# Optimization experiments

Measured on AMD Instinct MI355X. Metric: run time of the kernel, lower is better.

Reference implementation:

```python
import jax, jax.numpy as jnp
import numpy as np

K = 1024
D = 64
BETA = 0.25


def setup_inputs() -> dict:
    key = jax.random.key(0)
    k1, k2 = jax.random.split(key)
    latents = jax.random.normal(k1, (32, 64, 64, 64), dtype=jnp.float32)  # [B, C=D, H, W]
    # embedding init: uniform(-1/K, 1/K)
    embedding = jax.random.uniform(k2, (K, D), dtype=jnp.float32, minval=-1.0 / K, maxval=1.0 / K)
    return {"latents": latents, "embedding": embedding}


def reference(latents, embedding):
    # [B, D, H, W] -> [B, H, W, D]
    x = jnp.transpose(latents, (0, 2, 3, 1))
    shp = x.shape
    flat = x.reshape(-1, D)  # [N, D]

    dist = (jnp.sum(flat ** 2, axis=1, keepdims=True)
            + jnp.sum(embedding ** 2, axis=1)
            - 2.0 * flat @ embedding.T)  # [N, K]
    inds = jnp.argmin(dist, axis=1)  # [N]

    quantized = embedding[inds].reshape(shp)  # gather == one-hot @ embedding

    commitment_loss = jnp.mean((jax.lax.stop_gradient(quantized) - x) ** 2)
    embedding_loss = jnp.mean((quantized - jax.lax.stop_gradient(x)) ** 2)
    vq_loss = commitment_loss * BETA + embedding_loss

    # straight-through estimator
    quantized = x + jax.lax.stop_gradient(quantized - x)
    out = jnp.transpose(quantized, (0, 3, 1, 2))  # back to [B, D, H, W]
    return out, vq_loss
```

## Files before the change

kernel.cpp:

```cpp
#include <hip/hip_runtime.h>
#include <hip/hip_bf16.h>


#define HW 4096
#define OUTELEMS 8388608

typedef __attribute__((ext_vector_type(8))) short bf16x8;
typedef __attribute__((ext_vector_type(4))) float f32x4;

static __device__ __forceinline__ short f2bf(float f) {
    union { __hip_bfloat16 h; short s; } u;
    u.h = __float2bfloat16(f);
    return u.s;
}


__global__ __launch_bounds__(256) void prep_kernel(const float* __restrict__ emb,
                                                   short* __restrict__ Ebf,
                                                   float* __restrict__ en1,
                                                   float* __restrict__ embT,
                                                   float* __restrict__ loss) {
    int code = blockIdx.x * 4 + (threadIdx.x >> 6);
    int d = threadIdx.x & 63;
    float v = emb[code * 64 + d];
    int g = d >> 3, j = d & 7;
    Ebf[code * 64 + ((g + code) & 7) * 8 + j] = f2bf(-2.0f * v);
    embT[d * 1024 + code] = v;
    float s = v * v;
#pragma unroll
    for (int off = 32; off > 0; off >>= 1) s += __shfl_xor(s, off, 64);
    if (d == 0) en1[code] = 1.0f + s;
    if (blockIdx.x == 0 && threadIdx.x == 0) *loss = 0.0f;
}

__global__ __launch_bounds__(512, 4) void argmin_kernel(
        const float* __restrict__ lat, const short* __restrict__ Ebf,
        const float* __restrict__ en1, int* __restrict__ idx_out,
        float* __restrict__ loss) {
    __shared__ __align__(16) char sbuf[65536];
    const int tid  = threadIdx.x;
    const int wave = tid >> 6;
    const int lane = tid & 63;
    const int n    = lane & 15;
    const int quad = lane >> 4;

    const int g0 = blockIdx.x * 256;
    const int b  = g0 >> 12;
    const int m0 = (g0 & 4095) + wave * 32;
    const float* latb = lat + (size_t)b * 262144;
    const char* EbfB = (const char*)Ebf;

    f32x4 stg[4];
#pragma unroll
    for (int r = 0; r < 4; ++r)
        stg[r] = *(const f32x4*)(EbfB + r * 8192 + tid * 16);

    bf16x8 bfr[2][2];
    float xnorm[2];
    {
        float xv[32];
#pragma unroll
        for (int s = 0; s < 2; ++s) {
            const float* xp = latb + m0 + s * 16 + n;
#pragma unroll
            for (int j = 0; j < 8; ++j) {
                xv[s * 16 + j]     = xp[(quad * 8 + j) * HW];
                xv[s * 16 + 8 + j] = xp[(32 + quad * 8 + j) * HW];
            }
        }
#pragma unroll
        for (int s = 0; s < 2; ++s) {
            float xs = 0.0f; bf16x8 f0, f1;
#pragma unroll
            for (int j = 0; j < 8; ++j) {
                float x0 = xv[s * 16 + j], x1 = xv[s * 16 + 8 + j];
                xs += x0 * x0 + x1 * x1;
                f0[j] = f2bf(x0); f1[j] = f2bf(x1);
            }
            bfr[s][0] = f0; bfr[s][1] = f1; xnorm[s] = xs;
        }
    }

#pragma unroll
    for (int r = 0; r < 4; ++r)
        *(f32x4*)(sbuf + r * 8192 + tid * 16) = stg[r];
    __syncthreads();

    const f32x4* en1v = (const f32x4*)en1;
    unsigned emin[2] = {0xFFFFFFFFu, 0xFFFFFFFFu};
    const int slot0 = ((quad + n) & 7) * 16;
    const int slot1 = ((quad + 4 + n) & 7) * 16;

    for (int c = 0; c < 4; ++c) {
        const char* bufc = sbuf + (c & 1) * 32768;
        char* bufn = sbuf + ((c + 1) & 1) * 32768;
        if (c < 3) {
            const char* src = EbfB + (c + 1) * 32768;
#pragma unroll
            for (int r = 0; r < 4; ++r)
                stg[r] = *(const f32x4*)(src + r * 8192 + tid * 16);
        }
        const char* arow0 = bufc + n * 128 + slot0;
        const char* arow1 = bufc + n * 128 + slot1;
#pragma unroll 4
        for (int ctl = 0; ctl < 16; ++ctl) {
            bf16x8 a0 = *(const bf16x8*)(arow0 + ctl * 2048);
            bf16x8 a1 = *(const bf16x8*)(arow1 + ctl * 2048);
            f32x4 en4 = en1v[c * 64 + ctl * 4 + quad];
            f32x4 acc[2];
#pragma unroll
            for (int s = 0; s < 2; ++s)
                acc[s] = __builtin_amdgcn_mfma_f32_16x16x32_bf16(a0, bfr[s][0], en4, 0, 0, 0);
#pragma unroll
            for (int s = 0; s < 2; ++s)
                acc[s] = __builtin_amdgcn_mfma_f32_16x16x32_bf16(a1, bfr[s][1], acc[s], 0, 0, 0);
            const unsigned cb = c * 256 + ctl * 16 + quad * 4;
#pragma unroll
            for (int s = 0; s < 2; ++s) {
#pragma unroll
                for (int r = 0; r < 4; ++r) {
                    unsigned enc = (__float_as_uint(acc[s][r]) & 0xFFFFFC00u) | (cb + r);
                    emin[s] = enc < emin[s] ? enc : emin[s];
                }
            }
        }
        if (c < 3) {
#pragma unroll
            for (int r = 0; r < 4; ++r)
                *(f32x4*)(bufn + r * 8192 + tid * 16) = stg[r];
        }
        __syncthreads();
    }

#pragma unroll
    for (int off = 16; off <= 32; off <<= 1) {
#pragma unroll
        for (int s = 0; s < 2; ++s) {
            unsigned eo = (unsigned)__shfl_xor((int)emin[s], off, 64);
            float xo = __shfl_xor(xnorm[s], off, 64);
            emin[s] = eo < emin[s] ? eo : emin[s];
            xnorm[s] += xo;
        }
    }
    if (quad == 0) {
#pragma unroll
        for (int s = 0; s < 2; ++s)
            idx_out[b * HW + m0 + s * 16 + n] = (int)(emin[s] & 1023u);
    }
    float contrib = 0.0f;
#pragma unroll
    for (int s = 0; s < 2; ++s)
        contrib += __uint_as_float(emin[s] & 0xFFFFFC00u) - 1.0f + xnorm[s];
#pragma unroll
    for (int off = 32; off > 0; off >>= 1) contrib += __shfl_xor(contrib, off, 64);
    float* wsum = (float*)sbuf;
    if (lane == 0) wsum[wave] = contrib;
    __syncthreads();
    if (tid == 0) {
        float t = 0.0f;
#pragma unroll
        for (int w = 0; w < 8; ++w) t += wsum[w];
        atomicAdd(loss, t * (1.25f / (8388608.0f * 4.0f)));
    }
}

__global__ __launch_bounds__(256) void gather_kernel(const float* __restrict__ embT,
                                                     const int* __restrict__ idxb,
                                                     float* __restrict__ out) {
    int id = blockIdx.x * 256 + threadIdx.x;
    int m  = id & 4095;
    int d  = (id >> 12) & 63;
    int bbase = (id >> 18) << 12;
    int code = idxb[bbase + m];
    out[id] = embT[(d << 10) + code];
}

extern "C" void kernel_launch(void* const* d_in, const int* in_sizes, int n_in,
                              void* d_out, int out_size, void* d_ws, size_t ws_size,
                              hipStream_t stream) {
    const float* latents   = (const float*)d_in[0];
    const float* embedding = (const float*)d_in[1];
    float* out  = (float*)d_out;
    float* loss = out + OUTELEMS;

    char* ws = (char*)d_ws;
    short* Ebf   = (short*)ws;
    float* en1   = (float*)(ws + 131072);
    float* embT  = (float*)(ws + 135168);
    int*   idxb  = (int*)(ws + 397312);

    prep_kernel<<<256, 256, 0, stream>>>(embedding, Ebf, en1, embT, loss);
    argmin_kernel<<<512, 512, 0, stream>>>(latents, Ebf, en1, idxb, loss);
    gather_kernel<<<32768, 256, 0, stream>>>(embT, idxb, out);
}
```

Before: 120.1 us.

## Fuse codebook gather into argmin kernel with whole codebook resident in LDS

The separate gather kernel and the transposed fp32 embedding copy are removed. Each 1024-thread block now loads the entire bf16 codebook and the norms into about 134 KB of dynamic LDS once. It runs all 64 code tiles without double buffering, keeps the chosen codes in LDS, and writes the output directly from the LDS codebook with vectorised stores. This removes the index round trip through global memory, one kernel launch and the random embT reads. In exchange the output values are rebuilt from the bf16-rounded -2*e copy, which loses fp32 precision. The large LDS footprint also limits each CU to a single big block, which reduces latency hiding.

```diff
diff --git a/kernel.cpp b/kernel.cpp
--- a/kernel.cpp
+++ b/kernel.cpp
@@ -7,25 +7,27 @@
 
 typedef __attribute__((ext_vector_type(8))) short bf16x8;
 typedef __attribute__((ext_vector_type(4))) float f32x4;
+typedef __attribute__((ext_vector_type(4))) int i32x4;
 
 static __device__ __forceinline__ short f2bf(float f) {
     union { __hip_bfloat16 h; short s; } u;
     u.h = __float2bfloat16(f);
     return u.s;
 }
+static __device__ __forceinline__ unsigned umin2(unsigned a, unsigned b) {
+    return a < b ? a : b;
+}
 
 
 __global__ __launch_bounds__(256) void prep_kernel(const float* __restrict__ emb,
                                                    short* __restrict__ Ebf,
                                                    float* __restrict__ en1,
-                                                   float* __restrict__ embT,
                                                    float* __restrict__ loss) {
     int code = blockIdx.x * 4 + (threadIdx.x >> 6);
     int d = threadIdx.x & 63;
     float v = emb[code * 64 + d];
     int g = d >> 3, j = d & 7;
     Ebf[code * 64 + ((g + code) & 7) * 8 + j] = f2bf(-2.0f * v);
-    embT[d * 1024 + code] = v;
     float s = v * v;
 #pragma unroll
     for (int off = 32; off > 0; off >>= 1) s += __shfl_xor(s, off, 64);
@@ -33,103 +35,76 @@
     if (blockIdx.x == 0 && threadIdx.x == 0) *loss = 0.0f;
 }
 
-__global__ __launch_bounds__(512, 4) void argmin_kernel(
+__global__ __launch_bounds__(1024, 4) void vq_kernel(
         const float* __restrict__ lat, const short* __restrict__ Ebf,
-        const float* __restrict__ en1, int* __restrict__ idx_out,
+        const float* __restrict__ en1, float* __restrict__ out,
         float* __restrict__ loss) {
-    __shared__ __align__(16) char sbuf[65536];
+    extern __shared__ __align__(16) char sbuf[];
     const int tid  = threadIdx.x;
     const int wave = tid >> 6;
     const int lane = tid & 63;
     const int n    = lane & 15;
     const int quad = lane >> 4;
 
-    const int g0 = blockIdx.x * 256;
+    const int g0 = blockIdx.x * 512;
     const int b  = g0 >> 12;
-    const int m0 = (g0 & 4095) + wave * 32;
+    const int mb = g0 & 4095;
     const float* latb = lat + (size_t)b * 262144;
-    const char* EbfB = (const char*)Ebf;
 
-    f32x4 stg[4];
+    {
+        const f32x4* src = (const f32x4*)Ebf;
+        f32x4* dst = (f32x4*)sbuf;
 #pragma unroll
-    for (int r = 0; r < 4; ++r)
-        stg[r] = *(const f32x4*)(EbfB + r * 8192 + tid * 16);
+        for (int r = 0; r < 8; ++r)
+            dst[r * 1024 + tid] = src[r * 1024 + tid];
+        if (tid < 256)
+            ((f32x4*)(sbuf + 131072))[tid] = ((const f32x4*)en1)[tid];
+    }
 
     bf16x8 bfr[2][2];
     float xnorm[2];
-    {
-        float xv[32];
 #pragma unroll
-        for (int s = 0; s < 2; ++s) {
-            const float* xp = latb + m0 + s * 16 + n;
+    for (int s = 0; s < 2; ++s) {
+        const float* xp = latb + (mb + wave * 32 + s * 16 + n);
+        float xs = 0.0f; bf16x8 f0, f1;
 #pragma unroll
-            for (int j = 0; j < 8; ++j) {
-                xv[s * 16 + j]     = xp[(quad * 8 + j) * HW];
-                xv[s * 16 + 8 + j] = xp[(32 + quad * 8 + j) * HW];
-            }
+        for (int j = 0; j < 8; ++j) {
+            float x0 = xp[(quad * 8 + j) * HW];
+            float x1 = xp[(32 + quad * 8 + j) * HW];
+            xs += x0 * x0 + x1 * x1;
+            f0[j] = f2bf(x0); f1[j] = f2bf(x1);
         }
-#pragma unroll
-        for (int s = 0; s < 2; ++s) {
-            float xs = 0.0f; bf16x8 f0, f1;
-#pragma unroll
-            for (int j = 0; j < 8; ++j) {
-                float x0 = xv[s * 16 + j], x1 = xv[s * 16 + 8 + j];
-                xs += x0 * x0 + x1 * x1;
-                f0[j] = f2bf(x0); f1[j] = f2bf(x1);
-            }
-            bfr[s][0] = f0; bfr[s][1] = f1; xnorm[s] = xs;
-        }
+        bfr[s][0] = f0; bfr[s][1] = f1; xnorm[s] = xs;
     }
-
-#pragma unroll
-    for (int r = 0; r < 4; ++r)
-        *(f32x4*)(sbuf + r * 8192 + tid * 16) = stg[r];
     __syncthreads();
 
-    const f32x4* en1v = (const f32x4*)en1;
-    unsigned emin[2] = {0xFFFFFFFFu, 0xFFFFFFFFu};
     const int slot0 = ((quad + n) & 7) * 16;
     const int slot1 = ((quad + 4 + n) & 7) * 16;
+    const char* arowBase = sbuf + n * 128;
+    const f32x4* enl = (const f32x4*)(sbuf + 131072);
+    unsigned emin[2] = {0xFFFFFFFFu, 0xFFFFFFFFu};
 
-    for (int c = 0; c < 4; ++c) {
-        const char* bufc = sbuf + (c & 1) * 32768;
-        char* bufn = sbuf + ((c + 1) & 1) * 32768;
-        if (c < 3) {
-            const char* src = EbfB + (c + 1) * 32768;
-#pragma unroll
-            for (int r = 0; r < 4; ++r)
-                stg[r] = *(const f32x4*)(src + r * 8192 + tid * 16);
-        }
-        const char* arow0 = bufc + n * 128 + slot0;
-        const char* arow1 = bufc + n * 128 + slot1;
-#pragma unroll 4
-        for (int ctl = 0; ctl < 16; ++ctl) {
-            bf16x8 a0 = *(const bf16x8*)(arow0 + ctl * 2048);
-            bf16x8 a1 = *(const bf16x8*)(arow1 + ctl * 2048);
-            f32x4 en4 = en1v[c * 64 + ctl * 4 + quad];
-            f32x4 acc[2];
-#pragma unroll
-            for (int s = 0; s < 2; ++s)
-                acc[s] = __builtin_amdgcn_mfma_f32_16x16x32_bf16(a0, bfr[s][0], en4, 0, 0, 0);
-#pragma unroll
-            for (int s = 0; s < 2; ++s)
-                acc[s] = __builtin_amdgcn_mfma_f32_16x16x32_bf16(a1, bfr[s][1], acc[s], 0, 0, 0);
-            const unsigned cb = c * 256 + ctl * 16 + quad * 4;
-#pragma unroll
-            for (int s = 0; s < 2; ++s) {
-#pragma unroll
-                for (int r = 0; r < 4; ++r) {
-                    unsigned enc = (__float_as_uint(acc[s][r]) & 0xFFFFFC00u) | (cb + r);
-                    emin[s] = enc < emin[s] ? enc : emin[s];
-                }
-            }
-        }
-        if (c < 3) {
-#pragma unroll
-            for (int r = 0; r < 4; ++r)
-                *(f32x4*)(bufn + r * 8192 + tid * 16) = stg[r];
-        }
-        __syncthreads();
+#pragma unroll 2
+    for (int ct = 0; ct < 64; ++ct) {
+        const char* rb = arowBase + ct * 2048;
+        bf16x8 a0 = *(const bf16x8*)(rb + slot0);
+        bf16x8 a1 = *(const bf16x8*)(rb + slot1);
+        f32x4 en4 = enl[ct * 4 + quad];
+        f32x4 acc0 = __builtin_amdgcn_mfma_f32_16x16x32_bf16(a0, bfr[0][0], en4, 0, 0, 0);
+        f32x4 acc1 = __builtin_amdgcn_mfma_f32_16x16x32_bf16(a0, bfr[1][0], en4, 0, 0, 0);
+        acc0 = __builtin_amdgcn_mfma_f32_16x16x32_bf16(a1, bfr[0][1], acc0, 0, 0, 0);
+        acc1 = __builtin_amdgcn_mfma_f32_16x16x32_bf16(a1, bfr[1][1], acc1, 0, 0, 0);
+        const unsigned cb = ct * 16 + quad * 4;
+        unsigned e0 = (__float_as_uint(acc0[0]) & 0xFFFFFC00u) | (cb + 0);
+        unsigned e1 = (__float_as_uint(acc0[1]) & 0xFFFFFC00u) | (cb + 1);
+        unsigned e2 = (__float_as_uint(acc0[2]) & 0xFFFFFC00u) | (cb + 2);
+        unsigned e3 = (__float_as_uint(acc0[3]) & 0xFFFFFC00u) | (cb + 3);
+        emin[0] = umin2(emin[0], umin2(umin2(e0, e1), umin2(e2, e3)));
+        unsigned f0 = (__float_as_uint(acc1[0]) & 0xFFFFFC00u) | (cb + 0);
+        unsigned f1 = (__float_as_uint(acc1[1]) & 0xFFFFFC00u) | (cb + 1);
+        unsigned f2 = (__float_as_uint(acc1[2]) & 0xFFFFFC00u) | (cb + 2);
+        unsigned f3 = (__float_as_uint(acc1[3]) & 0xFFFFFC00u) | (cb + 3);
+        emin[1] = umin2(emin[1], umin2(umin2(f0, f1), umin2(f2, f3)));
     }
 
 #pragma unroll
@@ -142,37 +117,48 @@
             xnorm[s] += xo;
         }
     }
+
+    int* codes = (int*)(sbuf + 135168);
     if (quad == 0) {
-#pragma unroll
-        for (int s = 0; s < 2; ++s)
-            idx_out[b * HW + m0 + s * 16 + n] = (int)(emin[s] & 1023u);
+        codes[wave * 32 + n]      = (int)(emin[0] & 1023u);
+        codes[wave * 32 + 16 + n] = (int)(emin[1] & 1023u);
     }
+
     float contrib = 0.0f;
 #pragma unroll
     for (int s = 0; s < 2; ++s)
         contrib += __uint_as_float(emin[s] & 0xFFFFFC00u) - 1.0f + xnorm[s];
 #pragma unroll
     for (int off = 32; off > 0; off >>= 1) contrib += __shfl_xor(contrib, off, 64);
-    float* wsum = (float*)sbuf;
+    float* wsum = (float*)(sbuf + 137216);
     if (lane == 0) wsum[wave] = contrib;
     __syncthreads();
     if (tid == 0) {
         float t = 0.0f;
 #pragma unroll
-        for (int w = 0; w < 8; ++w) t += wsum[w];
+        for (int w = 0; w < 16; ++w) t += wsum[w];
         atomicAdd(loss, t * (1.25f / (8388608.0f * 4.0f)));
     }
-}
 
-__global__ __launch_bounds__(256) void gather_kernel(const float* __restrict__ embT,
-                                                     const int* __restrict__ idxb,
-                                                     float* __restrict__ out) {
-    int id = blockIdx.x * 256 + threadIdx.x;
-    int m  = id & 4095;
-    int d  = (id >> 12) & 63;
-    int bbase = (id >> 18) << 12;
-    int code = idxb[bbase + m];
-    out[id] = embT[(d << 10) + code];
+    float* outb = out + (size_t)b * 262144 + mb;
+#pragma unroll 2
+    for (int i = 0; i < 8; ++i) {
+        int id = i * 1024 + tid;
+        int d  = id >> 7;
+        int mq = (id & 127) * 4;
+        i32x4 c4 = *(const i32x4*)(codes + mq);
+        int g = d >> 3, j2 = (d & 7) * 2;
+        unsigned u0 = *(const unsigned short*)(sbuf + c4.x * 128 + ((g + c4.x) & 7) * 16 + j2);
+        unsigned u1 = *(const unsigned short*)(sbuf + c4.y * 128 + ((g + c4.y) & 7) * 16 + j2);
+        unsigned u2 = *(const unsigned short*)(sbuf + c4.z * 128 + ((g + c4.z) & 7) * 16 + j2);
+        unsigned u3 = *(const unsigned short*)(sbuf + c4.w * 128 + ((g + c4.w) & 7) * 16 + j2);
+        f32x4 v;
+        v[0] = __uint_as_float(u0 << 16) * -0.5f;
+        v[1] = __uint_as_float(u1 << 16) * -0.5f;
+        v[2] = __uint_as_float(u2 << 16) * -0.5f;
+        v[3] = __uint_as_float(u3 << 16) * -0.5f;
+        *(f32x4*)(outb + d * HW + mq) = v;
+    }
 }
 
 extern "C" void kernel_launch(void* const* d_in, const int* in_sizes, int n_in,
@@ -184,12 +170,12 @@
     float* loss = out + OUTELEMS;
 
     char* ws = (char*)d_ws;
-    short* Ebf   = (short*)ws;
-    float* en1   = (float*)(ws + 131072);
-    float* embT  = (float*)(ws + 135168);
-    int*   idxb  = (int*)(ws + 397312);
+    short* Ebf = (short*)ws;
+    float* en1 = (float*)(ws + 131072);
 
-    prep_kernel<<<256, 256, 0, stream>>>(embedding, Ebf, en1, embT, loss);
-    argmin_kernel<<<512, 512, 0, stream>>>(latents, Ebf, en1, idxb, loss);
-    gather_kernel<<<32768, 256, 0, stream>>>(embT, idxb, out);
+    hipFuncSetAttribute((const void*)vq_kernel,
+                        hipFuncAttributeMaxDynamicSharedMemorySize, 137280);
+
+    prep_kernel<<<256, 256, 0, stream>>>(embedding, Ebf, en1, loss);
+    vq_kernel<<<256, 1024, 137280, stream>>>(latents, Ebf, en1, out, loss);
 }
```

After: 106.2 us. 11.5% less time.
